# Performance work log

Hardware: AMD Instinct MI355X
Metric: run time of the kernel (lower is better)

## Reference

```python
import jax, jax.numpy as jnp
import numpy as np

N_TREES, DEPTH, INPUT_DIM, N_CLASSES = 15, 3, 128, 10
N_LEAVES = 2 ** DEPTH
N_INTERNAL = N_LEAVES - 1


def _path_masks(depth):
    """Right/left ancestor indicator matrices [n_leaves, n_internal]."""
    n_leaves = 2 ** depth
    n_int = n_leaves - 1
    R = np.zeros((n_leaves, n_int), np.float32)
    L = np.zeros((n_leaves, n_int), np.float32)
    for leaf in range(n_leaves):
        node = leaf + n_int
        for _ in range(depth):
            parent = (node - 1) // 2
            if node % 2 == 0:
                R[leaf, parent] = 1.0
            else:
                L[leaf, parent] = 1.0
            node = parent
    return R, L

_R, _L = _path_masks(DEPTH)


def setup_inputs() -> dict:
    key = jax.random.key(0)
    k1, k2 = jax.random.split(key)
    batch = 262144
    per_tree = N_INTERNAL * INPUT_DIM + N_INTERNAL + N_LEAVES * N_CLASSES
    total = N_TREES * per_tree + N_TREES
    x = jax.random.normal(k1, (batch, INPUT_DIM), dtype=jnp.float32)
    params = jax.random.normal(k2, (total,), dtype=jnp.float32)
    return {"x": x, "params": params}


def reference(x, params):
    per_tree = N_INTERNAL * INPUT_DIM + N_INTERNAL + N_LEAVES * N_CLASSES
    blocks = params[: N_TREES * per_tree].reshape(N_TREES, per_tree)
    w_end = N_INTERNAL * INPUT_DIM
    split_w = blocks[:, :w_end].reshape(N_TREES, N_INTERNAL, INPUT_DIM)
    split_b = blocks[:, w_end : w_end + N_INTERNAL]  # [T, n_internal]
    leaf_logits = blocks[:, w_end + N_INTERNAL :].reshape(N_TREES, N_LEAVES, N_CLASSES)
    tree_w_logits = params[N_TREES * per_tree :]  # [T]

    # split logits z: [B, T, n_internal]
    z = jnp.einsum("bd,tnd->btn", x, split_w) + split_b[None, :, :]
    log_p = jax.nn.log_sigmoid(z)        # log sigma(z)
    log_1mp = jax.nn.log_sigmoid(-z)     # log (1 - sigma(z))

    R = jnp.asarray(_R)
    L = jnp.asarray(_L)
    # path product in log domain: [B, T, n_leaves]
    leaf_probs = jnp.exp(
        jnp.einsum("btn,ln->btl", log_p, R) + jnp.einsum("btn,ln->btl", log_1mp, L)
    )

    leaf_class_probs = jax.nn.softmax(leaf_logits, axis=-1)  # [T, n_leaves, C]
    tree_pred = jnp.einsum("btl,tlc->btc", leaf_probs, leaf_class_probs)
    tree_weights = jax.nn.softmax(tree_w_logits, axis=0)     # [T]
    final_pred = jnp.einsum("btc,t->bc", tree_pred, tree_weights)
    return final_pred
```

## Files before the change

kernel.cpp:

```cpp
#include <hip/hip_runtime.h>
#include <hip/hip_fp16.h>


typedef float    f32x4 __attribute__((ext_vector_type(4)));
typedef _Float16 half8 __attribute__((ext_vector_type(8)));

#define TREES      15
#define IDIM       128
#define NCLS       10
#define NINT       7
#define NLVS       8
#define PER_TREE   (NINT*IDIM + NINT + NLVS*NCLS)
#define NODES      (TREES*NINT)
#define NPAD       112
#define KPAD       128
#define RSTR       272
#define QSTR       1040
#define QSZ        (8 * QSTR)
#define NBLK       512

__global__ __launch_bounds__(256) void prep_kernel(const float* __restrict__ p,
                                                   _Float16* __restrict__ wq,
                                                   float* __restrict__ bq,
                                                   _Float16* __restrict__ wbT) {
    const int gid  = blockIdx.x * 256 + threadIdx.x;
    const int nthr = gridDim.x * 256;

    for (int i = gid; i < NPAD * IDIM; i += nthr) {
        int g = i >> 7, k = i & 127;
        float v = 0.f;
        if (g < NODES) {
            int t = g / NINT, n = g % NINT;
            v = p[t * PER_TREE + n * IDIM + k];
        }
        wq[i] = (_Float16)v;
    }
    for (int i = gid; i < NPAD; i += nthr) {
        float v = 0.f;
        if (i < NODES) {
            int t = i / NINT, n = i % NINT;
            v = p[t * PER_TREE + NINT * IDIM + n];
        }
        bq[i] = v;
    }
    const float* tl = p + TREES * PER_TREE;
    for (int i = gid; i < 16 * KPAD; i += nthr) {
        int c = i >> 7, k = i & 127;
        float v = 0.f;
        if (c < NCLS && k < TREES * NLVS) {
            int t = k >> 3, l = k & 7;
            const float* ll = p + t * PER_TREE + NINT * IDIM + NINT + l * NCLS;
            float mx = ll[0];
            #pragma unroll
            for (int j = 1; j < NCLS; ++j) mx = fmaxf(mx, ll[j]);
            float se = 0.f;
            #pragma unroll
            for (int j = 0; j < NCLS; ++j) se += __expf(ll[j] - mx);
            float lsm = __expf(ll[c] - mx) / se;

            float m2 = tl[0];
            #pragma unroll
            for (int j = 1; j < TREES; ++j) m2 = fmaxf(m2, tl[j]);
            float s2 = 0.f;
            #pragma unroll
            for (int j = 0; j < TREES; ++j) s2 += __expf(tl[j] - m2);
            float tw = __expf(tl[t] - m2) / s2;
            v = lsm * tw;
        }
        wbT[i] = (_Float16)v;
    }
}

__device__ __forceinline__ void dma_quarter(const float* __restrict__ x,
                                            long grow0, char* qdst, int lane) {
    #pragma unroll
    for (int it = 0; it < 8; ++it) {
        const float* gp = x + (grow0 + 2 * it + (lane >> 5)) * IDIM + (lane & 31) * 4;
        __builtin_amdgcn_global_load_lds(
            (const __attribute__((address_space(1))) void*)gp,
            (__attribute__((address_space(3))) void*)(qdst + it * QSTR),
            16, 0, 0);
    }
}

__global__ __launch_bounds__(256, 2) void tree_main(const float* __restrict__ x,
                                                    const _Float16* __restrict__ wq,
                                                    const float* __restrict__ bq,
                                                    const _Float16* __restrict__ wbT,
                                                    float* __restrict__ out,
                                                    int tpb) {
    __shared__ __align__(16) char ldsA[4 * QSZ];
    __shared__ __align__(16) char ldsB[4 * QSZ];

    const int tid  = threadIdx.x;
    const int lane = tid & 63;
    const int w    = tid >> 6;
    const int lm   = lane & 15;
    const int lq   = lane >> 4;
    const int rg   = lane >> 2;
    const int g    = lane & 3;

    char* qA = &ldsA[w * QSZ];
    char* qB = &ldsB[w * QSZ];

    const long tile0 = (long)blockIdx.x * tpb;

    dma_quarter(x, tile0 * 64 + 16 * w, qA, lane);

    half8 bf[7][4];
    float bb[7];
    #pragma unroll
    for (int nt = 0; nt < 7; ++nt) {
        bb[nt] = bq[16 * nt + lm];
        #pragma unroll
        for (int s = 0; s < 4; ++s)
            bf[nt][s] = *reinterpret_cast<const half8*>(wq + (16 * nt + lm) * IDIM + 32 * s + 8 * lq);
    }
    half8 wbf[4];
    #pragma unroll
    for (int s = 0; s < 4; ++s)
        wbf[s] = *reinterpret_cast<const half8*>(wbT + lm * KPAD + 32 * s + 8 * lq);

    auto gather = [&](const char* q, half8 af[4]) {
        #pragma unroll
        for (int s = 0; s < 4; ++s) {
            const char* p0 = q + (lm >> 1) * QSTR + (lm & 1) * 512 + 128 * s + 32 * lq;
            f32x4 f0 = *(const f32x4*)(p0);
            f32x4 f1 = *(const f32x4*)(p0 + 16);
            half8 a;
            #pragma unroll
            for (int j = 0; j < 4; ++j) {
                a[j]     = (_Float16)f0[j];
                a[j + 4] = (_Float16)f1[j];
            }
            af[s] = a;
        }
    };

    auto compute = [&](char* q, const half8 af[4], long grow) {
        #pragma unroll
        for (int nt = 0; nt < 7; ++nt) {
            f32x4 acc = {0.f, 0.f, 0.f, 0.f};
            #pragma unroll
            for (int s = 0; s < 4; ++s)
                acc = __builtin_amdgcn_mfma_f32_16x16x32_f16(af[s], bf[nt][s], acc, 0, 0, 0);
            int node = 16 * nt + lm;
            int col  = node + ((node * 9363) >> 16);
            #pragma unroll
            for (int r = 0; r < 4; ++r) {
                float z  = acc[r] + bb[nt];
                float sg = __builtin_amdgcn_rcpf(1.0f + __expf(-z));
                *(_Float16*)(q + (4 * lq + r) * RSTR + col * 2) = (_Float16)sg;
            }
        }

        {
            const char* rowp = q + rg * RSTR;
            float sgv[4][7];
            #pragma unroll
            for (int tt = 0; tt < 4; ++tt) {
                #pragma unroll
                for (int n = 0; n < 7; ++n)
                    sgv[tt][n] = (float)*(const _Float16*)(rowp + (8 * (4 * g + tt) + n) * 2);
            }
            half8 lv[4];
            #pragma unroll
            for (int tt = 0; tt < 4; ++tt) {
                float s0 = sgv[tt][0], s1 = sgv[tt][1], s2 = sgv[tt][2];
                float s3 = sgv[tt][3], s4 = sgv[tt][4], s5 = sgv[tt][5], s6 = sgv[tt][6];
                float u1 = 1.f - s0, u2 = s0;
                float q1 = u1 * s1, q0 = u1 - q1;
                float q3 = u2 * s2, q2 = u2 - q3;
                float L1 = q0 * s3, L0 = q0 - L1;
                float L3 = q1 * s4, L2 = q1 - L3;
                float L5 = q2 * s5, L4 = q2 - L5;
                float L7 = q3 * s6, L6 = q3 - L7;
                float m = (4 * g + tt < TREES) ? 1.f : 0.f;
                half8 lv8;
                lv8[0] = (_Float16)(L0 * m); lv8[1] = (_Float16)(L1 * m);
                lv8[2] = (_Float16)(L2 * m); lv8[3] = (_Float16)(L3 * m);
                lv8[4] = (_Float16)(L4 * m); lv8[5] = (_Float16)(L5 * m);
                lv8[6] = (_Float16)(L6 * m); lv8[7] = (_Float16)(L7 * m);
                lv[tt] = lv8;
            }
            #pragma unroll
            for (int tt = 0; tt < 4; ++tt)
                *(half8*)(q + rg * RSTR + 64 * g + 16 * tt) = lv[tt];
        }

        {
            half8 af2[4];
            #pragma unroll
            for (int s = 0; s < 4; ++s)
                af2[s] = *(const half8*)(q + lm * RSTR + 64 * s + 16 * lq);
            f32x4 a2 = {0.f, 0.f, 0.f, 0.f};
            #pragma unroll
            for (int s = 0; s < 4; ++s)
                a2 = __builtin_amdgcn_mfma_f32_16x16x32_f16(af2[s], wbf[s], a2, 0, 0, 0);
            if (lm < NCLS) {
                #pragma unroll
                for (int r = 0; r < 4; ++r)
                    out[(grow + 16 * w + 4 * lq + r) * NCLS + lm] = a2[r];
            }
        }
    };

    for (int i = 0; i < tpb; i += 2) {
        half8 af[4];
        gather(qA, af);
        dma_quarter(x, (tile0 + i + 1) * 64 + 16 * w, qB, lane);
        compute(qA, af, (tile0 + i) * 64);

        gather(qB, af);
        if (i + 2 < tpb)
            dma_quarter(x, (tile0 + i + 2) * 64 + 16 * w, qA, lane);
        compute(qB, af, (tile0 + i + 1) * 64);
    }
}

extern "C" void kernel_launch(void* const* d_in, const int* in_sizes, int n_in,
                              void* d_out, int out_size, void* d_ws, size_t ws_size,
                              hipStream_t stream) {
    const float* x      = (const float*)d_in[0];
    const float* params = (const float*)d_in[1];
    float* out = (float*)d_out;

    _Float16* wq  = (_Float16*)d_ws;
    float*    bq  = (float*)((char*)d_ws + NPAD * IDIM * 2);
    _Float16* wbT = (_Float16*)((char*)bq + NPAD * 4);

    const int batch = in_sizes[0] / IDIM;
    const int tiles = batch / 64;
    const int tpb   = tiles / NBLK;

    prep_kernel<<<8, 256, 0, stream>>>(params, wq, bq, wbT);
    tree_main<<<NBLK, 256, 0, stream>>>(x, wq, bq, wbT, out, tpb);
}
```

Measured before the change: 204.8 us.

## Load x directly into registers with double-buffered prefetch instead of LDS DMA

Result: no change. 206.3 us (+0.7%).

```diff
diff --git a/kernel.cpp b/kernel.cpp
--- a/kernel.cpp
+++ b/kernel.cpp
@@ -2,8 +2,9 @@
 #include <hip/hip_fp16.h>
 
 
-typedef float    f32x4 __attribute__((ext_vector_type(4)));
-typedef _Float16 half8 __attribute__((ext_vector_type(8)));
+typedef float    f32x4  __attribute__((ext_vector_type(4)));
+typedef _Float16 half8  __attribute__((ext_vector_type(8)));
+typedef __fp16   fp16x2 __attribute__((ext_vector_type(2)));
 
 #define TREES      15
 #define IDIM       128
@@ -15,9 +16,8 @@
 #define NPAD       112
 #define KPAD       128
 #define RSTR       272
-#define QSTR       1040
-#define QSZ        (8 * QSTR)
 #define NBLK       512
+#define TPB        8
 
 __global__ __launch_bounds__(256) void prep_kernel(const float* __restrict__ p,
                                                    _Float16* __restrict__ wq,
@@ -71,26 +71,12 @@
     }
 }
 
-__device__ __forceinline__ void dma_quarter(const float* __restrict__ x,
-                                            long grow0, char* qdst, int lane) {
-    #pragma unroll
-    for (int it = 0; it < 8; ++it) {
-        const float* gp = x + (grow0 + 2 * it + (lane >> 5)) * IDIM + (lane & 31) * 4;
-        __builtin_amdgcn_global_load_lds(
-            (const __attribute__((address_space(1))) void*)gp,
-            (__attribute__((address_space(3))) void*)(qdst + it * QSTR),
-            16, 0, 0);
-    }
-}
-
 __global__ __launch_bounds__(256, 2) void tree_main(const float* __restrict__ x,
                                                     const _Float16* __restrict__ wq,
                                                     const float* __restrict__ bq,
                                                     const _Float16* __restrict__ wbT,
-                                                    float* __restrict__ out,
-                                                    int tpb) {
-    __shared__ __align__(16) char ldsA[4 * QSZ];
-    __shared__ __align__(16) char ldsB[4 * QSZ];
+                                                    float* __restrict__ out) {
+    __shared__ __align__(16) char lds[4][16 * RSTR];
 
     const int tid  = threadIdx.x;
     const int lane = tid & 63;
@@ -100,12 +86,9 @@
     const int rg   = lane >> 2;
     const int g    = lane & 3;
 
-    char* qA = &ldsA[w * QSZ];
-    char* qB = &ldsB[w * QSZ];
-
-    const long tile0 = (long)blockIdx.x * tpb;
-
-    dma_quarter(x, tile0 * 64 + 16 * w, qA, lane);
+    char* q = &lds[w][0];
+
+    const long tile0 = (long)blockIdx.x * TPB;
 
     half8 bf[7][4];
     float bb[7];
@@ -121,23 +104,33 @@
     for (int s = 0; s < 4; ++s)
         wbf[s] = *reinterpret_cast<const half8*>(wbT + lm * KPAD + 32 * s + 8 * lq);
 
-    auto gather = [&](const char* q, half8 af[4]) {
+    f32x4 P0[8], P1[8];
+    auto ldx = [&](f32x4 P[8], long tile) {
+        const float* xr = x + ((tile << 6) + 16 * w + lm) * IDIM + 8 * lq;
         #pragma unroll
         for (int s = 0; s < 4; ++s) {
-            const char* p0 = q + (lm >> 1) * QSTR + (lm & 1) * 512 + 128 * s + 32 * lq;
-            f32x4 f0 = *(const f32x4*)(p0);
-            f32x4 f1 = *(const f32x4*)(p0 + 16);
+            P[2 * s]     = *reinterpret_cast<const f32x4*>(xr + 32 * s);
+            P[2 * s + 1] = *reinterpret_cast<const f32x4*>(xr + 32 * s + 4);
+        }
+    };
+
+    auto cvt = [&](const f32x4 P[8], half8 af[4]) {
+        #pragma unroll
+        for (int s = 0; s < 4; ++s) {
+            fp16x2 h0 = __builtin_amdgcn_cvt_pkrtz(P[2*s][0],   P[2*s][1]);
+            fp16x2 h1 = __builtin_amdgcn_cvt_pkrtz(P[2*s][2],   P[2*s][3]);
+            fp16x2 h2 = __builtin_amdgcn_cvt_pkrtz(P[2*s+1][0], P[2*s+1][1]);
+            fp16x2 h3 = __builtin_amdgcn_cvt_pkrtz(P[2*s+1][2], P[2*s+1][3]);
             half8 a;
-            #pragma unroll
-            for (int j = 0; j < 4; ++j) {
-                a[j]     = (_Float16)f0[j];
-                a[j + 4] = (_Float16)f1[j];
-            }
+            a[0] = (_Float16)h0[0]; a[1] = (_Float16)h0[1];
+            a[2] = (_Float16)h1[0]; a[3] = (_Float16)h1[1];
+            a[4] = (_Float16)h2[0]; a[5] = (_Float16)h2[1];
+            a[6] = (_Float16)h3[0]; a[7] = (_Float16)h3[1];
             af[s] = a;
         }
     };
 
-    auto compute = [&](char* q, const half8 af[4], long grow) {
+    auto compute = [&](const half8 af[4], long tile) {
         #pragma unroll
         for (int nt = 0; nt < 7; ++nt) {
             f32x4 acc = {0.f, 0.f, 0.f, 0.f};
@@ -156,18 +149,16 @@
 
         {
             const char* rowp = q + rg * RSTR;
-            float sgv[4][7];
+            half8 sv[4];
+            #pragma unroll
+            for (int tt = 0; tt < 4; ++tt)
+                sv[tt] = *(const half8*)(rowp + (8 * (4 * g + tt)) * 2);
+            half8 lv[4];
             #pragma unroll
             for (int tt = 0; tt < 4; ++tt) {
-                #pragma unroll
-                for (int n = 0; n < 7; ++n)
-                    sgv[tt][n] = (float)*(const _Float16*)(rowp + (8 * (4 * g + tt) + n) * 2);
-            }
-            half8 lv[4];
-            #pragma unroll
-            for (int tt = 0; tt < 4; ++tt) {
-                float s0 = sgv[tt][0], s1 = sgv[tt][1], s2 = sgv[tt][2];
-                float s3 = sgv[tt][3], s4 = sgv[tt][4], s5 = sgv[tt][5], s6 = sgv[tt][6];
+                float s0 = (float)sv[tt][0], s1 = (float)sv[tt][1], s2 = (float)sv[tt][2];
+                float s3 = (float)sv[tt][3], s4 = (float)sv[tt][4], s5 = (float)sv[tt][5];
+                float s6 = (float)sv[tt][6];
                 float u1 = 1.f - s0, u2 = s0;
                 float q1 = u1 * s1, q0 = u1 - q1;
                 float q3 = u2 * s2, q2 = u2 - q3;
@@ -198,23 +189,24 @@
             for (int s = 0; s < 4; ++s)
                 a2 = __builtin_amdgcn_mfma_f32_16x16x32_f16(af2[s], wbf[s], a2, 0, 0, 0);
             if (lm < NCLS) {
+                const long grow = (tile << 6) + 16 * w;
                 #pragma unroll
                 for (int r = 0; r < 4; ++r)
-                    out[(grow + 16 * w + 4 * lq + r) * NCLS + lm] = a2[r];
+                    out[(grow + 4 * lq + r) * NCLS + lm] = a2[r];
             }
         }
     };
 
-    for (int i = 0; i < tpb; i += 2) {
+    ldx(P0, tile0 + 0);
+    ldx(P1, tile0 + 1);
+    for (int i = 0; i < TPB; i += 2) {
         half8 af[4];
-        gather(qA, af);
-        dma_quarter(x, (tile0 + i + 1) * 64 + 16 * w, qB, lane);
-        compute(qA, af, (tile0 + i) * 64);
-
-        gather(qB, af);
-        if (i + 2 < tpb)
-            dma_quarter(x, (tile0 + i + 2) * 64 + 16 * w, qA, lane);
-        compute(qB, af, (tile0 + i + 1) * 64);
+        cvt(P0, af);
+        if (i + 2 < TPB) ldx(P0, tile0 + i + 2);
+        compute(af, tile0 + i);
+        cvt(P1, af);
+        if (i + 3 < TPB) ldx(P1, tile0 + i + 3);
+        compute(af, tile0 + i + 1);
     }
 }
 
@@ -229,10 +221,6 @@
     float*    bq  = (float*)((char*)d_ws + NPAD * IDIM * 2);
     _Float16* wbT = (_Float16*)((char*)bq + NPAD * 4);
 
-    const int batch = in_sizes[0] / IDIM;
-    const int tiles = batch / 64;
-    const int tpb   = tiles / NBLK;
-
     prep_kernel<<<8, 256, 0, stream>>>(params, wq, bq, wbT);
-    tree_main<<<NBLK, 256, 0, stream>>>(x, wq, bq, wbT, out, tpb);
+    tree_main<<<NBLK, 256, 0, stream>>>(x, wq, bq, wbT, out);
 }
```
